# Kernel optimization log

Hardware: AMD Instinct MI355X
Metric: run time of the kernel (lower is better)

## Reference

```python
import jax, jax.numpy as jnp
import numpy as np

N_NODES = 100000
N_EDGES = 1600000
IN_C, HID_C, OUT_C = 128, 128, 64


def setup_inputs() -> dict:
    key = jax.random.key(0)
    k1, k2, k3, k4 = jax.random.split(key, 4)
    x = jax.random.normal(k1, (N_NODES, IN_C), dtype=jnp.float32)
    edge_index = jax.random.randint(k2, (2, N_EDGES), 0, N_NODES, dtype=jnp.int32)
    # Glorot-style init scale for the linear weights (matches PyG GCNConv default)
    W1 = jax.random.normal(k3, (IN_C, HID_C), dtype=jnp.float32) * (1.0 / np.sqrt(IN_C))
    b1 = jnp.zeros((HID_C,), dtype=jnp.float32)
    W2 = jax.random.normal(k4, (HID_C, OUT_C), dtype=jnp.float32) * (1.0 / np.sqrt(HID_C))
    b2 = jnp.zeros((OUT_C,), dtype=jnp.float32)
    return {"x": x, "edge_index": edge_index, "W1": W1, "b1": b1, "W2": W2, "b2": b2}


def _gcn_norm(edge_index, num_nodes):
    """Add self-loops and compute symmetric normalization deg^-1/2[src]*deg^-1/2[dst]."""
    src, dst = edge_index[0], edge_index[1]
    loop = jnp.arange(num_nodes, dtype=src.dtype)
    src_f = jnp.concatenate([src, loop])
    dst_f = jnp.concatenate([dst, loop])
    ones = jnp.ones_like(dst_f, dtype=jnp.float32)
    deg = jax.ops.segment_sum(ones, dst_f, num_segments=num_nodes)  # in-degree incl. self-loop
    deg_inv_sqrt = jnp.where(deg > 0, jax.lax.rsqrt(deg), 0.0)
    norm = deg_inv_sqrt[src_f] * deg_inv_sqrt[dst_f]  # [E+N]
    return src_f, dst_f, norm


def _gcn_conv(x, W, b, src_f, dst_f, norm, num_nodes):
    h = x @ W                              # [N, C_out] linear transform first
    msg = h[src_f] * norm[:, None]         # gather + scale, [E+N, C_out]
    agg = jax.ops.segment_sum(msg, dst_f, num_segments=num_nodes)  # scatter-add
    return agg + b


def reference(x, edge_index, W1, b1, W2, b2):
    n = x.shape[0]
    src_f, dst_f, norm = _gcn_norm(edge_index, n)
    h = jax.nn.relu(_gcn_conv(x, W1, b1, src_f, dst_f, norm, n))
    out = _gcn_conv(h, W2, b2, src_f, dst_f, norm, n)
    return out
```

## Files before the change

### kernel.cpp

```cpp
#include <hip/hip_runtime.h>


constexpr int BLK = 256;
constexpr int PCAP = 2560;
constexpr int CPAD = 16;
constexpr int CHUNK = 6144;
constexpr int NBMAX = 800;


__global__ __launch_bounds__(512)
void bucket_sort_kernel(const int* __restrict__ src, const int* __restrict__ dst,
                        int* __restrict__ bcnt, unsigned* __restrict__ ebuf,
                        int e, int nbuck) {
    __shared__ unsigned stage[CHUNK];
    __shared__ unsigned short keys[CHUNK];
    __shared__ int hist[NBMAX];
    __shared__ int excl[NBMAX];
    __shared__ int gbase[NBMAX];
    __shared__ int wsum[512];

    const int t = threadIdx.x;
    const int base = blockIdx.x * CHUNK;
    const int cnt = min(CHUNK, e - base);

    for (int i = t; i < nbuck; i += 512) hist[i] = 0;
    __syncthreads();

    for (int i = t; i < cnt; i += 512) atomicAdd(&hist[dst[base + i] >> 7], 1);
    __syncthreads();

    const int b0 = t * 2;
    int s0 = 0, s1 = 0;
    if (b0 < nbuck)     s0 = hist[b0];
    if (b0 + 1 < nbuck) s1 = hist[b0 + 1];
    wsum[t] = s0 + s1;
    __syncthreads();
    for (int off = 1; off < 512; off <<= 1) {
        int v = (t >= off) ? wsum[t - off] : 0;
        __syncthreads();
        wsum[t] += v;
        __syncthreads();
    }
    int run = (t > 0) ? wsum[t - 1] : 0;
    if (b0 < nbuck)     { excl[b0]     = run; hist[b0]     = run; run += s0; }
    if (b0 + 1 < nbuck) { excl[b0 + 1] = run; hist[b0 + 1] = run; run += s1; }
    __syncthreads();

    for (int i = t; i < cnt; i += 512) {
        int s = src[base + i], d = dst[base + i];
        int bb = d >> 7;
        int p = atomicAdd(&hist[bb], 1);
        stage[p] = ((unsigned)s << 7) | (unsigned)(d & 127);
        keys[p] = (unsigned short)bb;
    }
    __syncthreads();

    if (b0 < nbuck)     { int c = hist[b0]     - excl[b0];     gbase[b0]     = c ? atomicAdd(&bcnt[b0 * CPAD], c)       : 0; }
    if (b0 + 1 < nbuck) { int c = hist[b0 + 1] - excl[b0 + 1]; gbase[b0 + 1] = c ? atomicAdd(&bcnt[(b0 + 1) * CPAD], c) : 0; }
    __syncthreads();

    for (int i = t; i < cnt; i += 512) {
        int bb = keys[i];
        int p = gbase[bb] + (i - excl[bb]);
        if (p < PCAP) ebuf[(size_t)bb * PCAP + p] = stage[i];
    }
}


__global__ __launch_bounds__(256)
void build_kernel(const unsigned* __restrict__ ebuf, const int* __restrict__ bcnt,
                  float* __restrict__ dis, int2* __restrict__ rp,
                  int* __restrict__ esrc, int n) {
    __shared__ int packed[PCAP];
    __shared__ unsigned short rank[PCAP];
    __shared__ int hist[128];
    __shared__ int excl[128];
    __shared__ int start[128];

    const int b = blockIdx.x, t = threadIdx.x;
    const int base = b << 7;
    const int nloc = min(128, n - base);
    const int tot = min(bcnt[b * CPAD], PCAP);

    if (t < 128) hist[t] = 0;
    __syncthreads();

    const unsigned* eb = ebuf + (size_t)b * PCAP;
    for (int i = t; i < tot; i += 256) {
        int v = (int)eb[i];
        packed[i] = v;
        rank[i] = (unsigned short)atomicAdd(&hist[v & 127], 1);
    }
    __syncthreads();

    if (t < 128) excl[t] = hist[t];
    __syncthreads();
    for (int off = 1; off < 128; off <<= 1) {
        int v = (t >= off && t < 128) ? excl[t - off] : 0;
        __syncthreads();
        if (t < 128) excl[t] += v;
        __syncthreads();
    }

    if (t < 128) {
        int deg = hist[t];
        int st = excl[t] - deg;
        start[t] = st;
        if (t < nloc) {
            dis[base + t] = rsqrtf((float)(deg + 1));
            int gs = b * PCAP + st;
            rp[base + t] = make_int2(gs, gs + deg);
        }
    }
    __syncthreads();

    int* eo = esrc + b * PCAP;
    for (int i = t; i < tot; i += 256) {
        int v = packed[i];
        eo[start[v & 127] + rank[i]] = v >> 7;
    }
}


__device__ __forceinline__ unsigned short f2bf(float f) {
    unsigned u = __float_as_uint(f);
    u += 0x7fffu + ((u >> 16) & 1u);
    return (unsigned short)(u >> 16);
}
__device__ __forceinline__ float bflo(unsigned u) { return __uint_as_float(u << 16); }
__device__ __forceinline__ float bfhi(unsigned u) { return __uint_as_float(u & 0xffff0000u); }
__device__ __forceinline__ unsigned pk2(short a, short b) {
    return (unsigned)(unsigned short)a | ((unsigned)(unsigned short)b << 16);
}

__device__ __forceinline__ void split2(float v, short& hi, short& lo) {
    unsigned short h = f2bf(v);
    float hf = __uint_as_float(((unsigned)h) << 16);
    hi = (short)h;
    lo = (short)f2bf(v - hf);
}

typedef __attribute__((ext_vector_type(8))) short bf16x8;
typedef __attribute__((ext_vector_type(4))) float f32x4;
#define MFMA_B16(a, b, c) __builtin_amdgcn_mfma_f32_16x16x32_bf16(a, b, c, 0, 0, 0)

__device__ __forceinline__ void split8(const float4& a, const float4& b, bf16x8& h, bf16x8& l) {
    short hh, ll;
    split2(a.x, hh, ll); h[0] = hh; l[0] = ll;
    split2(a.y, hh, ll); h[1] = hh; l[1] = ll;
    split2(a.z, hh, ll); h[2] = hh; l[2] = ll;
    split2(a.w, hh, ll); h[3] = hh; l[3] = ll;
    split2(b.x, hh, ll); h[4] = hh; l[4] = ll;
    split2(b.y, hh, ll); h[5] = hh; l[5] = ll;
    split2(b.z, hh, ll); h[6] = hh; l[6] = ll;
    split2(b.w, hh, ll); h[7] = hh; l[7] = ll;
}


__global__ void prep_b_kernel(const float* __restrict__ W1, const float* __restrict__ W2,
                              unsigned short* __restrict__ B1h, unsigned short* __restrict__ B1l,
                              unsigned short* __restrict__ B2h, unsigned short* __restrict__ B2l) {
    const int c = blockIdx.x;
    const int k = threadIdx.x;
    short h, l;
    if (c < 128) {
        split2(W1[(size_t)k * 128 + c], h, l);
        B1h[c * 128 + k] = (unsigned short)h;
        B1l[c * 128 + k] = (unsigned short)l;
    } else {
        const int c2 = c - 128;
        split2(W2[(size_t)k * 64 + c2], h, l);
        B2h[c2 * 128 + k] = (unsigned short)h;
        B2l[c2 * 128 + k] = (unsigned short)l;
    }
}


constexpr int BAS = 72;

__global__ __launch_bounds__(256, 4)
void gemm_mfma(const float* __restrict__ Af,
               const unsigned short* __restrict__ Bh, const unsigned short* __restrict__ Bl,
               const float* __restrict__ dis, unsigned* __restrict__ Cb, int nrows) {
    constexpr int COLS = 128;
    constexpr int CT = COLS / 16;
    constexpr int BE = COLS * BAS;
    constexpr int CSC = COLS + 8;
    constexpr int SMEM = (2 * BE * 2 > 128 * CSC * 2) ? 2 * BE * 2 : 128 * CSC * 2;

    __shared__ __align__(16) char smem[SMEM];
    short* sBh = (short*)smem;
    short* sBl = sBh + BE;

    const int t = threadIdx.x;
    const int rowbase = blockIdx.x * 128;
    const int wave = t >> 6;
    const int lane = t & 63;
    const int quad = lane >> 4;
    const int l16 = lane & 15;

    const int gr0 = rowbase + wave * 32 + l16;
    const int gr1 = gr0 + 16;

    f32x4 acc[2][CT];
#pragma unroll
    for (int rt = 0; rt < 2; ++rt)
#pragma unroll
        for (int ct = 0; ct < CT; ++ct) {
            f32x4 z = {0.f, 0.f, 0.f, 0.f};
            acc[rt][ct] = z;
        }

    for (int half = 0; half < 2; ++half) {
        {
            constexpr int NV = COLS * 8;
            uint4* dh = (uint4*)sBh;
            uint4* dl = (uint4*)sBl;
            const uint4* gh = (const uint4*)Bh;
            const uint4* gl = (const uint4*)Bl;
            for (int idx = t; idx < NV; idx += 256) {
                int c = idx >> 3, kq = idx & 7;
                int gidx = c * 16 + half * 8 + kq;
                int didx = c * 9 + kq;
                dh[didx] = gh[gidx];
                dl[didx] = gl[gidx];
            }
        }
        __syncthreads();

#pragma unroll
        for (int kc = 0; kc < 2; ++kc) {
            const int ko = kc * 32 + quad * 8;
            bf16x8 ah0, al0, ah1, al1;
            float4 va = {0.f, 0.f, 0.f, 0.f}, vb = va, vc = va, vd = va;
            if (gr0 < nrows) {
                const float4* ap = (const float4*)(Af + (size_t)gr0 * 128 + half * 64 + ko);
                va = ap[0]; vb = ap[1];
            }
            if (gr1 < nrows) {
                const float4* ap = (const float4*)(Af + (size_t)gr1 * 128 + half * 64 + ko);
                vc = ap[0]; vd = ap[1];
            }
            split8(va, vb, ah0, al0);
            split8(vc, vd, ah1, al1);
#pragma unroll
            for (int ct = 0; ct < CT; ++ct) {
                const int bo = (ct * 16 + l16) * BAS + ko;
                bf16x8 bh = *(const bf16x8*)&sBh[bo];
                bf16x8 bl = *(const bf16x8*)&sBl[bo];
                acc[0][ct] = MFMA_B16(ah0, bh, acc[0][ct]);
                acc[1][ct] = MFMA_B16(ah1, bh, acc[1][ct]);
                acc[0][ct] = MFMA_B16(al0, bh, acc[0][ct]);
                acc[1][ct] = MFMA_B16(al1, bh, acc[1][ct]);
                acc[0][ct] = MFMA_B16(ah0, bl, acc[0][ct]);
                acc[1][ct] = MFMA_B16(ah1, bl, acc[1][ct]);
            }
        }
        __syncthreads();
    }

    short* Cs = (short*)smem;
    float sv[2][4];
#pragma unroll
    for (int rt = 0; rt < 2; ++rt)
#pragma unroll
        for (int r = 0; r < 4; ++r) {
            int rr = rowbase + wave * 32 + rt * 16 + quad * 4 + r;
            sv[rt][r] = (rr < nrows) ? dis[rr] : 0.f;
        }
#pragma unroll
    for (int rt = 0; rt < 2; ++rt)
#pragma unroll
        for (int ct = 0; ct < CT; ++ct) {
            const int rb = wave * 32 + rt * 16 + quad * 4;
            const int c = ct * 16 + l16;
#pragma unroll
            for (int r = 0; r < 4; ++r)
                Cs[(rb + r) * CSC + c] = (short)f2bf(sv[rt][r] * acc[rt][ct][r]);
        }
    __syncthreads();

    {
        const int row = t >> 1, hf = t & 1;
        const int gr = rowbase + row;
        if (gr < nrows) {
            const uint4* cr = (const uint4*)&Cs[row * CSC + hf * (COLS / 2)];
            uint4* dstp = (uint4*)Cb + (size_t)gr * (COLS / 8) + hf * (COLS / 16);
#pragma unroll
            for (int i = 0; i < COLS / 16; ++i) dstp[i] = cr[i];
        }
    }
}


#define ACC8(v)                                           \
    acc[0] += bflo(v.x); acc[1] += bfhi(v.x);             \
    acc[2] += bflo(v.y); acc[3] += bfhi(v.y);             \
    acc[4] += bflo(v.z); acc[5] += bfhi(v.z);             \
    acc[6] += bflo(v.w); acc[7] += bfhi(v.w);

__global__ __launch_bounds__(512)
void gather_gemm_kernel(const int2* __restrict__ rp, const int* __restrict__ esrc,
                        const float* __restrict__ dis, const unsigned* __restrict__ hs,
                        const float* __restrict__ bias,
                        const unsigned short* __restrict__ B2h,
                        const unsigned short* __restrict__ B2l,
                        unsigned* __restrict__ h2b, int n) {
    constexpr int ASTR = 136;
    constexpr int CSTR = 72;
    __shared__ __align__(16) short sAh[32 * ASTR];
    __shared__ __align__(16) short sAl[32 * ASTR];

    const int t = threadIdx.x;
    const int base = blockIdx.x * 32;

    {
        const int nl = t >> 4;
        const int lc = t & 15;
        const int node = base + nl;

        if (node < n) {
            const uint4* h4 = (const uint4*)hs;
            const int2 se = rp[node];
            float acc[8];
            {
                uint4 v = h4[(size_t)node * 16 + lc];
                acc[0] = bflo(v.x); acc[1] = bfhi(v.x);
                acc[2] = bflo(v.y); acc[3] = bfhi(v.y);
                acc[4] = bflo(v.z); acc[5] = bfhi(v.z);
                acc[6] = bflo(v.w); acc[7] = bfhi(v.w);
            }
            int k = se.x;
            const int end = se.y;
            for (; k + 3 < end; k += 4) {
                int s0 = esrc[k], s1 = esrc[k + 1], s2 = esrc[k + 2], s3 = esrc[k + 3];
                uint4 v0 = h4[(size_t)s0 * 16 + lc];
                uint4 v1 = h4[(size_t)s1 * 16 + lc];
                uint4 v2 = h4[(size_t)s2 * 16 + lc];
                uint4 v3 = h4[(size_t)s3 * 16 + lc];
                ACC8(v0) ACC8(v1) ACC8(v2) ACC8(v3)
            }
            for (; k < end; ++k) {
                uint4 v = h4[(size_t)esrc[k] * 16 + lc];
                ACC8(v)
            }

            const float di = dis[node];
            const float4 ba = ((const float4*)bias)[lc * 2];
            const float4 bb = ((const float4*)bias)[lc * 2 + 1];
            float v0 = fmaxf(fmaf(di, acc[0], ba.x), 0.f);
            float v1 = fmaxf(fmaf(di, acc[1], ba.y), 0.f);
            float v2 = fmaxf(fmaf(di, acc[2], ba.z), 0.f);
            float v3 = fmaxf(fmaf(di, acc[3], ba.w), 0.f);
            float v4 = fmaxf(fmaf(di, acc[4], bb.x), 0.f);
            float v5 = fmaxf(fmaf(di, acc[5], bb.y), 0.f);
            float v6 = fmaxf(fmaf(di, acc[6], bb.z), 0.f);
            float v7 = fmaxf(fmaf(di, acc[7], bb.w), 0.f);

            short h0, l0, h1, l1, h2, l2, h3, l3, h4v, l4, h5, l5, h6, l6, h7, l7;
            split2(v0, h0, l0); split2(v1, h1, l1); split2(v2, h2, l2); split2(v3, h3, l3);
            split2(v4, h4v, l4); split2(v5, h5, l5); split2(v6, h6, l6); split2(v7, h7, l7);
            uint4 oh, ol;
            oh.x = pk2(h0, h1); oh.y = pk2(h2, h3); oh.z = pk2(h4v, h5); oh.w = pk2(h6, h7);
            ol.x = pk2(l0, l1); ol.y = pk2(l2, l3); ol.z = pk2(l4, l5);  ol.w = pk2(l6, l7);
            *(uint4*)&sAh[nl * ASTR + lc * 8] = oh;
            *(uint4*)&sAl[nl * ASTR + lc * 8] = ol;
        } else {
            uint4 z = {0u, 0u, 0u, 0u};
            *(uint4*)&sAh[nl * ASTR + lc * 8] = z;
            *(uint4*)&sAl[nl * ASTR + lc * 8] = z;
        }
    }
    __syncthreads();

    const int wave = t >> 6, lane = t & 63, quad = lane >> 4, l16 = lane & 15;
    const int col = wave * 16 + l16;
    f32x4 c0 = {0.f, 0.f, 0.f, 0.f}, c1 = c0;
    if (t < 256) {
#pragma unroll
        for (int ks = 0; ks < 4; ++ks) {
            const int ko = ks * 32 + quad * 8;
            bf16x8 bh = *(const bf16x8*)&B2h[col * 128 + ko];
            bf16x8 bl = *(const bf16x8*)&B2l[col * 128 + ko];
            bf16x8 ah0 = *(const bf16x8*)&sAh[l16 * ASTR + ko];
            bf16x8 al0 = *(const bf16x8*)&sAl[l16 * ASTR + ko];
            bf16x8 ah1 = *(const bf16x8*)&sAh[(16 + l16) * ASTR + ko];
            bf16x8 al1 = *(const bf16x8*)&sAl[(16 + l16) * ASTR + ko];
            c0 = MFMA_B16(ah0, bh, c0);
            c1 = MFMA_B16(ah1, bh, c1);
            c0 = MFMA_B16(al0, bh, c0);
            c1 = MFMA_B16(al1, bh, c1);
            c0 = MFMA_B16(ah0, bl, c0);
            c1 = MFMA_B16(ah1, bl, c1);
        }
    }
    __syncthreads();

    short* Cs = sAh;
    if (t < 256) {
#pragma unroll
        for (int r = 0; r < 4; ++r) {
            const int row0 = quad * 4 + r, row1 = 16 + quad * 4 + r;
            const float d0 = (base + row0 < n) ? dis[base + row0] : 0.f;
            const float d1 = (base + row1 < n) ? dis[base + row1] : 0.f;
            Cs[row0 * CSTR + col] = (short)f2bf(d0 * c0[r]);
            Cs[row1 * CSTR + col] = (short)f2bf(d1 * c1[r]);
        }
    }
    __syncthreads();
    if (t < 256) {
        const int row = t >> 3, l8 = t & 7;
        const int gr = base + row;
        if (gr < n)
            ((uint4*)h2b)[(size_t)gr * 8 + l8] = *(const uint4*)&Cs[row * CSTR + l8 * 8];
    }
}


#define ACCLO(v)                                          \
    acc[0] += bflo(v.x); acc[1] += bfhi(v.x);             \
    acc[2] += bflo(v.y); acc[3] += bfhi(v.y);             \
    acc[4] += bflo(v.z); acc[5] += bfhi(v.z);             \
    acc[6] += bflo(v.w); acc[7] += bfhi(v.w);
#define ACCHI(v)                                          \
    acc[8]  += bflo(v.x); acc[9]  += bfhi(v.x);           \
    acc[10] += bflo(v.y); acc[11] += bfhi(v.y);           \
    acc[12] += bflo(v.z); acc[13] += bfhi(v.z);           \
    acc[14] += bflo(v.w); acc[15] += bfhi(v.w);

__global__ __launch_bounds__(256)
void gather_out_kernel(const int2* __restrict__ rp, const int* __restrict__ esrc,
                       const float* __restrict__ dis, const unsigned* __restrict__ hs,
                       const float* __restrict__ bias, float* __restrict__ out, int n) {
    const int gid = blockIdx.x * BLK + threadIdx.x;
    const int node = gid >> 2;
    const int l4 = gid & 3;
    if (node >= n) return;

    const uint4* h4 = (const uint4*)hs;
    const int2 se = rp[node];

    float acc[16];
    {
        uint4 v0 = h4[(size_t)node * 8 + l4];
        uint4 v1 = h4[(size_t)node * 8 + 4 + l4];
        acc[0] = bflo(v0.x); acc[1] = bfhi(v0.x);
        acc[2] = bflo(v0.y); acc[3] = bfhi(v0.y);
        acc[4] = bflo(v0.z); acc[5] = bfhi(v0.z);
        acc[6] = bflo(v0.w); acc[7] = bfhi(v0.w);
        acc[8]  = bflo(v1.x); acc[9]  = bfhi(v1.x);
        acc[10] = bflo(v1.y); acc[11] = bfhi(v1.y);
        acc[12] = bflo(v1.z); acc[13] = bfhi(v1.z);
        acc[14] = bflo(v1.w); acc[15] = bfhi(v1.w);
    }

    int k = se.x;
    const int end = se.y;
    for (; k + 3 < end; k += 4) {
        int s0 = esrc[k], s1 = esrc[k + 1], s2 = esrc[k + 2], s3 = esrc[k + 3];
        uint4 a0 = h4[(size_t)s0 * 8 + l4], b0 = h4[(size_t)s0 * 8 + 4 + l4];
        uint4 a1 = h4[(size_t)s1 * 8 + l4], b1 = h4[(size_t)s1 * 8 + 4 + l4];
        uint4 a2 = h4[(size_t)s2 * 8 + l4], b2 = h4[(size_t)s2 * 8 + 4 + l4];
        uint4 a3 = h4[(size_t)s3 * 8 + l4], b3 = h4[(size_t)s3 * 8 + 4 + l4];
        ACCLO(a0) ACCHI(b0) ACCLO(a1) ACCHI(b1)
        ACCLO(a2) ACCHI(b2) ACCLO(a3) ACCHI(b3)
    }
    for (; k < end; ++k) {
        int s = esrc[k];
        uint4 a = h4[(size_t)s * 8 + l4], b = h4[(size_t)s * 8 + 4 + l4];
        ACCLO(a) ACCHI(b)
    }

    const float di = dis[node];
    const float4* b4 = (const float4*)bias;
    const float4 ba = b4[l4 * 2], bb = b4[l4 * 2 + 1];
    const float4 bc = b4[8 + l4 * 2], bd = b4[9 + l4 * 2];
    float4 o0, o1, o2, o3;
    o0.x = fmaf(di, acc[0],  ba.x); o0.y = fmaf(di, acc[1],  ba.y);
    o0.z = fmaf(di, acc[2],  ba.z); o0.w = fmaf(di, acc[3],  ba.w);
    o1.x = fmaf(di, acc[4],  bb.x); o1.y = fmaf(di, acc[5],  bb.y);
    o1.z = fmaf(di, acc[6],  bb.z); o1.w = fmaf(di, acc[7],  bb.w);
    o2.x = fmaf(di, acc[8],  bc.x); o2.y = fmaf(di, acc[9],  bc.y);
    o2.z = fmaf(di, acc[10], bc.z); o2.w = fmaf(di, acc[11], bc.w);
    o3.x = fmaf(di, acc[12], bd.x); o3.y = fmaf(di, acc[13], bd.y);
    o3.z = fmaf(di, acc[14], bd.z); o3.w = fmaf(di, acc[15], bd.w);
    float4* o4 = (float4*)out;
    o4[(size_t)node * 16 + l4 * 2]     = o0;
    o4[(size_t)node * 16 + l4 * 2 + 1] = o1;
    o4[(size_t)node * 16 + 8 + l4 * 2]     = o2;
    o4[(size_t)node * 16 + 8 + l4 * 2 + 1] = o3;
}

#undef ACC8
#undef ACCLO
#undef ACCHI


extern "C" void kernel_launch(void* const* d_in, const int* in_sizes, int n_in,
                              void* d_out, int out_size, void* d_ws, size_t ws_size,
                              hipStream_t stream) {
    const float* x  = (const float*)d_in[0];
    const int*   ei = (const int*)d_in[1];
    const float* W1 = (const float*)d_in[2];
    const float* b1 = (const float*)d_in[3];
    const float* W2 = (const float*)d_in[4];
    const float* b2 = (const float*)d_in[5];
    float* out = (float*)d_out;

    const int n = in_sizes[0] / 128;
    const int e = in_sizes[1] / 2;
    const int* src = ei;
    const int* dst = ei + e;

    char* ws = (char*)d_ws;
    float*    dis  = (float*)   (ws + 0x0);
    int2*     rp   = (int2*)    (ws + 0x80000);
    int*      bcnt = (int*)     (ws + 0x180000);
    unsigned short* B1h = (unsigned short*)(ws + 0x1A0000);
    unsigned short* B1l = (unsigned short*)(ws + 0x1A8000);
    unsigned short* B2h = (unsigned short*)(ws + 0x1B0000);
    unsigned short* B2l = (unsigned short*)(ws + 0x1B4000);
    int*      esrc = (int*)     (ws + 0x280000);
    unsigned* hb   = (unsigned*)(ws + 0xB00000);
    unsigned* h2b  = (unsigned*)(ws + 0x2400000);
    unsigned* ebuf = (unsigned*)(ws + 0x2400000);

    const int nbuck = (n + 127) >> 7;
    const int nb_g = (n + 127) / 128;

    hipMemsetAsync(bcnt, 0, (size_t)nbuck * CPAD * 4, stream);
    prep_b_kernel<<<192, 128, 0, stream>>>(W1, W2, B1h, B1l, B2h, B2l);
    bucket_sort_kernel<<<(e + CHUNK - 1) / CHUNK, 512, 0, stream>>>(src, dst, bcnt, ebuf, e, nbuck);
    build_kernel<<<nbuck, 256, 0, stream>>>(ebuf, bcnt, dis, rp, esrc, n);

    gemm_mfma<<<nb_g, 256, 0, stream>>>(x, B1h, B1l, dis, hb, n);

    gather_gemm_kernel<<<(n + 31) / 32, 512, 0, stream>>>(
        rp, esrc, dis, hb, b1, B2h, B2l, h2b, n);

    gather_out_kernel<<<(n * 4 + BLK - 1) / BLK, BLK, 0, stream>>>(
        rp, esrc, dis, h2b, b2, out, n);
}
```

Baseline: 263.6 us.

## Replace atomic bucket sort with count/scan/place pipeline and split second GEMM across waves

The single bucket-sort kernel, which claimed per-bucket global offsets with atomics, becomes three kernels: per-chunk histograms, a per-bucket scan across chunks, and a placement pass using the precomputed offsets. Chunk size drops to 2048 and blocks to 256 threads. This removes the memset and global atomics and makes placement deterministic. The cost is two extra launches and a count matrix round-trip through memory. Separately, the second GEMM stage now spreads its 32x64 output tile over all 8 waves, one 16x16 tile each, instead of 4 waves doing two tiles while the other 4 idle.

```diff
diff --git a/kernel.cpp b/kernel.cpp
--- a/kernel.cpp
+++ b/kernel.cpp
@@ -3,72 +3,138 @@
 
 constexpr int BLK = 256;
 constexpr int PCAP = 2560;
-constexpr int CPAD = 16;
-constexpr int CHUNK = 6144;
+constexpr int CHUNK = 2048;
 constexpr int NBMAX = 800;
 
 
-__global__ __launch_bounds__(512)
-void bucket_sort_kernel(const int* __restrict__ src, const int* __restrict__ dst,
-                        int* __restrict__ bcnt, unsigned* __restrict__ ebuf,
-                        int e, int nbuck) {
+__global__ __launch_bounds__(256)
+void count_kernel(const int* __restrict__ dst, unsigned short* __restrict__ cnt,
+                  int e, int nbuck) {
+    __shared__ int hist[NBMAX];
+    const int t = threadIdx.x;
+    const int base = blockIdx.x * CHUNK;
+    const int cend = min(CHUNK, e - base);
+
+    for (int i = t; i < nbuck; i += 256) hist[i] = 0;
+    __syncthreads();
+    for (int i = t; i < cend; i += 256) atomicAdd(&hist[dst[base + i] >> 7], 1);
+    __syncthreads();
+    unsigned short* o = cnt + (size_t)blockIdx.x * nbuck;
+    for (int i = t; i < nbuck; i += 256) o[i] = (unsigned short)hist[i];
+}
+
+
+__global__ __launch_bounds__(256)
+void scan_bins_kernel(unsigned short* __restrict__ cnt, int* __restrict__ totals,
+                      int nbuck, int nblk) {
+    __shared__ int wsum[256];
+    const int j = blockIdx.x;
+    const int t = threadIdx.x;
+    const int b0 = t * 4;
+    int v[4];
+    int s = 0;
+#pragma unroll
+    for (int q = 0; q < 4; ++q) {
+        const int B = b0 + q;
+        v[q] = (B < nblk) ? (int)cnt[(size_t)B * nbuck + j] : 0;
+        s += v[q];
+    }
+    wsum[t] = s;
+    __syncthreads();
+    for (int off = 1; off < 256; off <<= 1) {
+        int u = (t >= off) ? wsum[t - off] : 0;
+        __syncthreads();
+        wsum[t] += u;
+        __syncthreads();
+    }
+    int run = (t > 0) ? wsum[t - 1] : 0;
+#pragma unroll
+    for (int q = 0; q < 4; ++q) {
+        const int B = b0 + q;
+        if (B < nblk) {
+            cnt[(size_t)B * nbuck + j] = (unsigned short)min(run, PCAP);
+            run += v[q];
+        }
+    }
+    if (t == 255) totals[j] = run;
+}
+
+
+__global__ __launch_bounds__(256)
+void place_kernel(const int* __restrict__ src, const int* __restrict__ dst,
+                  const unsigned short* __restrict__ cnt, unsigned* __restrict__ ebuf,
+                  int e, int nbuck) {
     __shared__ unsigned stage[CHUNK];
     __shared__ unsigned short keys[CHUNK];
     __shared__ int hist[NBMAX];
     __shared__ int excl[NBMAX];
     __shared__ int gbase[NBMAX];
-    __shared__ int wsum[512];
+    __shared__ int wsum[256];
 
     const int t = threadIdx.x;
     const int base = blockIdx.x * CHUNK;
-    const int cnt = min(CHUNK, e - base);
-
-    for (int i = t; i < nbuck; i += 512) hist[i] = 0;
-    __syncthreads();
-
-    for (int i = t; i < cnt; i += 512) atomicAdd(&hist[dst[base + i] >> 7], 1);
-    __syncthreads();
-
-    const int b0 = t * 2;
-    int s0 = 0, s1 = 0;
+    const int cend = min(CHUNK, e - base);
+
+    for (int i = t; i < nbuck; i += 256) hist[i] = 0;
+    __syncthreads();
+
+    int dreg[8];
+#pragma unroll
+    for (int q = 0; q < 8; ++q) {
+        const int i = t + q * 256;
+        dreg[q] = (i < cend) ? dst[base + i] : -1;
+        if (i < cend) atomicAdd(&hist[dreg[q] >> 7], 1);
+    }
+    __syncthreads();
+
+    const int b0 = t * 4;
+    int s0 = 0, s1 = 0, s2 = 0, s3 = 0;
     if (b0 < nbuck)     s0 = hist[b0];
     if (b0 + 1 < nbuck) s1 = hist[b0 + 1];
-    wsum[t] = s0 + s1;
-    __syncthreads();
-    for (int off = 1; off < 512; off <<= 1) {
-        int v = (t >= off) ? wsum[t - off] : 0;
-        __syncthreads();
-        wsum[t] += v;
+    if (b0 + 2 < nbuck) s2 = hist[b0 + 2];
+    if (b0 + 3 < nbuck) s3 = hist[b0 + 3];
+    wsum[t] = s0 + s1 + s2 + s3;
+    __syncthreads();
+    for (int off = 1; off < 256; off <<= 1) {
+        int u = (t >= off) ? wsum[t - off] : 0;
+        __syncthreads();
+        wsum[t] += u;
         __syncthreads();
     }
     int run = (t > 0) ? wsum[t - 1] : 0;
     if (b0 < nbuck)     { excl[b0]     = run; hist[b0]     = run; run += s0; }
     if (b0 + 1 < nbuck) { excl[b0 + 1] = run; hist[b0 + 1] = run; run += s1; }
-    __syncthreads();
-
-    for (int i = t; i < cnt; i += 512) {
-        int s = src[base + i], d = dst[base + i];
-        int bb = d >> 7;
-        int p = atomicAdd(&hist[bb], 1);
-        stage[p] = ((unsigned)s << 7) | (unsigned)(d & 127);
-        keys[p] = (unsigned short)bb;
-    }
-    __syncthreads();
-
-    if (b0 < nbuck)     { int c = hist[b0]     - excl[b0];     gbase[b0]     = c ? atomicAdd(&bcnt[b0 * CPAD], c)       : 0; }
-    if (b0 + 1 < nbuck) { int c = hist[b0 + 1] - excl[b0 + 1]; gbase[b0 + 1] = c ? atomicAdd(&bcnt[(b0 + 1) * CPAD], c) : 0; }
-    __syncthreads();
-
-    for (int i = t; i < cnt; i += 512) {
-        int bb = keys[i];
-        int p = gbase[bb] + (i - excl[bb]);
+    if (b0 + 2 < nbuck) { excl[b0 + 2] = run; hist[b0 + 2] = run; run += s2; }
+    if (b0 + 3 < nbuck) { excl[b0 + 3] = run; hist[b0 + 3] = run; run += s3; }
+    {
+        const unsigned short* cb = cnt + (size_t)blockIdx.x * nbuck;
+        for (int i = t; i < nbuck; i += 256) gbase[i] = (int)cb[i];
+    }
+    __syncthreads();
+
+#pragma unroll
+    for (int q = 0; q < 8; ++q) {
+        const int i = t + q * 256;
+        if (i < cend) {
+            const int s = src[base + i], d = dreg[q];
+            const int bb = d >> 7;
+            const int p = atomicAdd(&hist[bb], 1);
+            stage[p] = ((unsigned)s << 7) | (unsigned)(d & 127);
+            keys[p] = (unsigned short)bb;
+        }
+    }
+    __syncthreads();
+
+    for (int i = t; i < cend; i += 256) {
+        const int bb = keys[i];
+        const int p = gbase[bb] + (i - excl[bb]);
         if (p < PCAP) ebuf[(size_t)bb * PCAP + p] = stage[i];
     }
 }
 
 
 __global__ __launch_bounds__(256)
-void build_kernel(const unsigned* __restrict__ ebuf, const int* __restrict__ bcnt,
+void build_kernel(const unsigned* __restrict__ ebuf, const int* __restrict__ totals,
                   float* __restrict__ dis, int2* __restrict__ rp,
                   int* __restrict__ esrc, int n) {
     __shared__ int packed[PCAP];
@@ -80,7 +146,7 @@
     const int b = blockIdx.x, t = threadIdx.x;
     const int base = b << 7;
     const int nloc = min(128, n - base);
-    const int tot = min(bcnt[b * CPAD], PCAP);
+    const int tot = min(totals[b], PCAP);
 
     if (t < 128) hist[t] = 0;
     __syncthreads();
@@ -374,38 +440,30 @@
     __syncthreads();
 
     const int wave = t >> 6, lane = t & 63, quad = lane >> 4, l16 = lane & 15;
-    const int col = wave * 16 + l16;
-    f32x4 c0 = {0.f, 0.f, 0.f, 0.f}, c1 = c0;
-    if (t < 256) {
-#pragma unroll
-        for (int ks = 0; ks < 4; ++ks) {
-            const int ko = ks * 32 + quad * 8;
-            bf16x8 bh = *(const bf16x8*)&B2h[col * 128 + ko];
-            bf16x8 bl = *(const bf16x8*)&B2l[col * 128 + ko];
-            bf16x8 ah0 = *(const bf16x8*)&sAh[l16 * ASTR + ko];
-            bf16x8 al0 = *(const bf16x8*)&sAl[l16 * ASTR + ko];
-            bf16x8 ah1 = *(const bf16x8*)&sAh[(16 + l16) * ASTR + ko];
-            bf16x8 al1 = *(const bf16x8*)&sAl[(16 + l16) * ASTR + ko];
-            c0 = MFMA_B16(ah0, bh, c0);
-            c1 = MFMA_B16(ah1, bh, c1);
-            c0 = MFMA_B16(al0, bh, c0);
-            c1 = MFMA_B16(al1, bh, c1);
-            c0 = MFMA_B16(ah0, bl, c0);
-            c1 = MFMA_B16(ah1, bl, c1);
-        }
+    const int rt = wave & 1;
+    const int ct = wave >> 1;
+    const int col = ct * 16 + l16;
+    const int arow = (rt * 16 + l16) * ASTR;
+    f32x4 c0 = {0.f, 0.f, 0.f, 0.f};
+#pragma unroll
+    for (int ks = 0; ks < 4; ++ks) {
+        const int ko = ks * 32 + quad * 8;
+        bf16x8 bh = *(const bf16x8*)&B2h[col * 128 + ko];
+        bf16x8 bl = *(const bf16x8*)&B2l[col * 128 + ko];
+        bf16x8 ah = *(const bf16x8*)&sAh[arow + ko];
+        bf16x8 al = *(const bf16x8*)&sAl[arow + ko];
+        c0 = MFMA_B16(ah, bh, c0);
+        c0 = MFMA_B16(al, bh, c0);
+        c0 = MFMA_B16(ah, bl, c0);
     }
     __syncthreads();
 
     short* Cs = sAh;
-    if (t < 256) {
-#pragma unroll
-        for (int r = 0; r < 4; ++r) {
-            const int row0 = quad * 4 + r, row1 = 16 + quad * 4 + r;
-            const float d0 = (base + row0 < n) ? dis[base + row0] : 0.f;
-            const float d1 = (base + row1 < n) ? dis[base + row1] : 0.f;
-            Cs[row0 * CSTR + col] = (short)f2bf(d0 * c0[r]);
-            Cs[row1 * CSTR + col] = (short)f2bf(d1 * c1[r]);
-        }
+#pragma unroll
+    for (int r = 0; r < 4; ++r) {
+        const int row = rt * 16 + quad * 4 + r;
+        const float d = (base + row < n) ? dis[base + row] : 0.f;
+        Cs[row * CSTR + col] = (short)f2bf(d * c0[r]);
     }
     __syncthreads();
     if (t < 256) {
@@ -513,25 +571,28 @@
     const int* dst = ei + e;
 
     char* ws = (char*)d_ws;
-    float*    dis  = (float*)   (ws + 0x0);
-    int2*     rp   = (int2*)    (ws + 0x80000);
-    int*      bcnt = (int*)     (ws + 0x180000);
-    unsigned short* B1h = (unsigned short*)(ws + 0x1A0000);
-    unsigned short* B1l = (unsigned short*)(ws + 0x1A8000);
-    unsigned short* B2h = (unsigned short*)(ws + 0x1B0000);
-    unsigned short* B2l = (unsigned short*)(ws + 0x1B4000);
-    int*      esrc = (int*)     (ws + 0x280000);
+    float*    dis    = (float*)   (ws + 0x0);
+    int2*     rp     = (int2*)    (ws + 0x80000);
+    int*      totals = (int*)     (ws + 0x180000);
+    unsigned short* B1h = (unsigned short*)(ws + 0x182000);
+    unsigned short* B1l = (unsigned short*)(ws + 0x18A000);
+    unsigned short* B2h = (unsigned short*)(ws + 0x192000);
+    unsigned short* B2l = (unsigned short*)(ws + 0x196000);
+    unsigned short* cnt = (unsigned short*)(ws + 0x1A0000);
+    int*      esrc = (int*)     (ws + 0x2E0000);
     unsigned* hb   = (unsigned*)(ws + 0xB00000);
     unsigned* h2b  = (unsigned*)(ws + 0x2400000);
     unsigned* ebuf = (unsigned*)(ws + 0x2400000);
 
     const int nbuck = (n + 127) >> 7;
+    const int nblk = (e + CHUNK - 1) / CHUNK;
     const int nb_g = (n + 127) / 128;
 
-    hipMemsetAsync(bcnt, 0, (size_t)nbuck * CPAD * 4, stream);
     prep_b_kernel<<<192, 128, 0, stream>>>(W1, W2, B1h, B1l, B2h, B2l);
-    bucket_sort_kernel<<<(e + CHUNK - 1) / CHUNK, 512, 0, stream>>>(src, dst, bcnt, ebuf, e, nbuck);
-    build_kernel<<<nbuck, 256, 0, stream>>>(ebuf, bcnt, dis, rp, esrc, n);
+    count_kernel<<<nblk, 256, 0, stream>>>(dst, cnt, e, nbuck);
+    scan_bins_kernel<<<nbuck, 256, 0, stream>>>(cnt, totals, nbuck, nblk);
+    place_kernel<<<nblk, 256, 0, stream>>>(src, dst, cnt, ebuf, e, nbuck);
+    build_kernel<<<nbuck, 256, 0, stream>>>(ebuf, totals, dis, rp, esrc, n);
 
     gemm_mfma<<<nb_g, 256, 0, stream>>>(x, B1h, B1l, dis, hb, n);
 
```

Result: slower. 278.1 us (+5.5%).
